# Kernel optimization log

Measured on AMD Instinct MI355X. Metric: run time of the kernel, lower is better.

The kernel has to match this reference:

```python
import jax, jax.numpy as jnp
import numpy as np

DIM, E, K, H = 1024, 8, 2, 4096

def setup_inputs() -> dict:
    key = jax.random.key(0)
    ks = jax.random.split(key, 5)
    s_in = 1.0 / np.sqrt(DIM)
    s_h = 1.0 / np.sqrt(H)
    return {
        "x": jax.random.normal(ks[0], (4, 2048, DIM), dtype=jnp.float32),
        "Wr": jax.random.normal(ks[1], (DIM, E), dtype=jnp.float32) * s_in,
        "W1": jax.random.normal(ks[2], (E, DIM, H), dtype=jnp.float32) * s_in,
        "b1": jnp.zeros((E, H), dtype=jnp.float32),
        "W2": jax.random.normal(ks[3], (E, H, DIM), dtype=jnp.float32) * s_h,
        "b2": jnp.zeros((E, DIM), dtype=jnp.float32),
    }

def reference(x, Wr, W1, b1, W2, b2):
    batch, seq, dim = x.shape
    x_flat = x.reshape(-1, dim)                      # [T, D]
    logits = x_flat @ Wr                             # [T, E]
    w, ind = jax.lax.top_k(logits, K)                # [T, K]
    w = jax.nn.softmax(w, axis=-1)
    # combine[t, e] = sum_i w[t, i] * (ind[t, i] == e)
    combine = jnp.einsum('tke,tk->te', jax.nn.one_hot(ind, E, dtype=x.dtype), w)  # [T, E]

    def body(acc, params):
        W1e, b1e, W2e, b2e, ce = params
        h = jax.nn.gelu(x_flat @ W1e + b1e, approximate=False)  # exact GELU (torch nn.GELU default)
        y = h @ W2e + b2e                                        # [T, D]
        return acc + ce[:, None] * y, None

    out0 = jnp.zeros_like(x_flat)
    out, _ = jax.lax.scan(body, out0, (W1, b1, W2, b2, combine.T))
    return out.reshape(batch, seq, dim)
```

## Files before the change

### kernel.cpp

```cpp
#include <hip/hip_runtime.h>
#include <hip/hip_bf16.h>

#define TDIM 1024
#define NEXP 8
#define NHID 4096

typedef __hip_bfloat16 bf16;
typedef __attribute__((ext_vector_type(8))) short bf16x8;
typedef __attribute__((ext_vector_type(8))) unsigned short u16x8;
typedef __attribute__((ext_vector_type(4))) float f32x4;

__device__ __forceinline__ void gload_lds16(void* lds, const void* g) {
  __builtin_amdgcn_global_load_lds(
      (const __attribute__((address_space(1))) unsigned int*)g,
      (__attribute__((address_space(3))) unsigned int*)lds, 16, 0, 0);
}

__device__ __forceinline__ unsigned short f2bf_bits(float f) {
  __hip_bfloat16 b = __float2bfloat16(f);
  unsigned short u;
  __builtin_memcpy(&u, &b, 2);
  return u;
}

__device__ __forceinline__ float bf2f(unsigned short u) {
  union { unsigned int i; float f; } c;
  c.i = ((unsigned int)u) << 16;
  return c.f;
}

__device__ __forceinline__ void cvt_chunk(const float* __restrict__ src, bf16* __restrict__ dst,
                                          int c, int kqShift, int nMask, int rowLen) {
  const int kq = c >> kqShift;
  const int n = c & nMask;
  const float* s = src + ((size_t)kq * 8) * rowLen + n;
  u16x8 o;
#pragma unroll
  for (int j = 0; j < 8; ++j) o[j] = f2bf_bits(s[(size_t)j * rowLen]);
  *reinterpret_cast<u16x8*>(dst + (size_t)c * 8) = o;
}

__global__ __launch_bounds__(256) void prep_kernel(
    const float* __restrict__ W1, bf16* __restrict__ W1C, const float* __restrict__ W2,
    bf16* __restrict__ W2C, const float* __restrict__ x, bf16* __restrict__ xb,
    const float* __restrict__ Wr, int* __restrict__ idx, float* __restrict__ wtok,
    int* __restrict__ cnt, int T) {
  const int pb = blockIdx.x;
  const int tid = threadIdx.x;
  if (pb < 8192) {
    const int id = pb * 256 + tid;
    cvt_chunk(W1, W1C, id, 12, 4095, 4096);
    cvt_chunk(W1, W1C, id + (1 << 21), 12, 4095, 4096);
    cvt_chunk(W2, W2C, id, 10, 1023, 1024);
    cvt_chunk(W2, W2C, id + (1 << 21), 10, 1023, 1024);
  } else {
    const int p = pb - 8192;
    const int wave = p * 4 + (tid >> 6);
    const int lane = tid & 63;
    if (wave >= T) return;
    const float4* xr4 = reinterpret_cast<const float4*>(x + (size_t)wave * TDIM);
    bf16* xbrow = xb + (size_t)wave * TDIM;
    float acc[NEXP];
#pragma unroll
    for (int e = 0; e < NEXP; ++e) acc[e] = 0.f;
    const float4* wr4 = reinterpret_cast<const float4*>(Wr);
#pragma unroll
    for (int i = 0; i < TDIM / 256; ++i) {
      float4 xv = xr4[lane + i * 64];
      ushort4 o;
      o.x = f2bf_bits(xv.x);
      o.y = f2bf_bits(xv.y);
      o.z = f2bf_bits(xv.z);
      o.w = f2bf_bits(xv.w);
      *reinterpret_cast<ushort4*>(xbrow + (lane + i * 64) * 4) = o;
      int row = (lane + i * 64) * 4;
#pragma unroll
      for (int j = 0; j < 4; ++j) {
        float xs = (&xv.x)[j];
        float4 wa = wr4[(row + j) * 2];
        float4 wb = wr4[(row + j) * 2 + 1];
        acc[0] += xs * wa.x;
        acc[1] += xs * wa.y;
        acc[2] += xs * wa.z;
        acc[3] += xs * wa.w;
        acc[4] += xs * wb.x;
        acc[5] += xs * wb.y;
        acc[6] += xs * wb.z;
        acc[7] += xs * wb.w;
      }
    }
#pragma unroll
    for (int e = 0; e < NEXP; ++e) {
      float v = acc[e];
#pragma unroll
      for (int s = 32; s; s >>= 1) v += __shfl_xor(v, s);
      acc[e] = v;
    }
    if (lane == 0) {
      int e0 = 0;
      float l0 = acc[0];
      for (int e = 1; e < NEXP; ++e)
        if (acc[e] > l0) { l0 = acc[e]; e0 = e; }
      int e1 = -1;
      float l1 = -INFINITY;
      for (int e = 0; e < NEXP; ++e)
        if (e != e0 && acc[e] > l1) { l1 = acc[e]; e1 = e; }
      float z = __expf(l1 - l0);
      idx[wave * 2] = e0;
      idx[wave * 2 + 1] = e1;
      wtok[wave * 2] = 1.f / (1.f + z);
      wtok[wave * 2 + 1] = z / (1.f + z);
      atomicAdd(&cnt[e0], 1);
      atomicAdd(&cnt[e1], 1);
    }
  }
}

__global__ void scan_kernel(const int* __restrict__ cnt, int* __restrict__ offs) {
  if (threadIdx.x == 0 && blockIdx.x == 0) {
    int s = 0;
    for (int e = 0; e < NEXP; ++e) { offs[e] = s; s += cnt[e]; }
  }
}

__global__ void build_perm_kernel(const int* __restrict__ idx, const int* __restrict__ offs,
                                  int* __restrict__ fill, int* __restrict__ perm,
                                  int* __restrict__ islot, int T) {
  int t = blockIdx.x * blockDim.x + threadIdx.x;
  if (t >= T) return;
#pragma unroll
  for (int k = 0; k < 2; ++k) {
    int e = idx[t * 2 + k];
    int p = offs[e] + atomicAdd(&fill[e], 1);
    perm[p] = t;
    islot[t * 2 + k] = p;
  }
}

template <int KD, int ND, bool GATHER, bool GELU>
__global__ __launch_bounds__(512, 2) void moe_gemm8(
    const bf16* __restrict__ A, const bf16* __restrict__ BC, const float* __restrict__ bias,
    const int* __restrict__ perm, const int* __restrict__ cnt, const int* __restrict__ offs,
    bf16* __restrict__ Dst, int nm, int nn) {
  __shared__ short lds[65536];

  const int nwg = NEXP * nm * nn;
  const int bid = blockIdx.x;
  const int wg = (bid & 7) * (nwg >> 3) + (bid >> 3);
  const int e = wg / (nm * nn);
  const int rem = wg % (nm * nn);
  const int mb = rem / nn, nb = rem % nn;

  const int ce = cnt[e];
  const int m0 = mb * 256;
  if (m0 >= ce) return;
  const int base = offs[e];
  const int n0 = nb * 256;
  const int tid = threadIdx.x;
  const int lane = tid & 63;
  const int wid = tid >> 6;
  const int wm = wid >> 2, wn = wid & 3;
  const int lcol = lane & 15;
  const int lkg = (lane >> 4) * 8;

  const int kxs0 = ((lkg << 1) ^ ((lcol & 7) << 4)) >> 1;
  const int kxs1 = (((lkg + 32) << 1) ^ ((lcol & 7) << 4)) >> 1;
  int aRow[4], bRow[2];
#pragma unroll
  for (int mm = 0; mm < 4; ++mm) aRow[mm] = (wm * 64 + mm * 16 + lcol) << 6;
#pragma unroll
  for (int n2 = 0; n2 < 2; ++n2) bRow[n2] = (wn * 32 + n2 * 16 + lcol) << 6;

  const bf16* aP[2][2];
  const bf16* bP[2][2];
#pragma unroll
  for (int h = 0; h < 2; ++h)
#pragma unroll
    for (int i = 0; i < 2; ++i) {
      int s = tid + i * 512;
      int srow = s >> 3;
      int ksrc = (s & 7) ^ (srow & 7);
      int grow = m0 + h * 128 + srow;
      if (grow > ce - 1) grow = ce - 1;
      size_t arow = GATHER ? (size_t)perm[base + grow] : (size_t)(base + grow);
      aP[h][i] = A + arow * KD + ksrc * 8;
      bP[h][i] = BC + (size_t)e * KD * ND + ((size_t)ksrc * ND + (n0 + h * 128 + srow)) * 8;
    }

  f32x4 acc[8][4];
#pragma unroll
  for (int m = 0; m < 8; ++m)
#pragma unroll
    for (int n = 0; n < 4; ++n) acc[m][n] = (f32x4){0.f, 0.f, 0.f, 0.f};

  bf16x8 fA[4][2], fB[2][2];

#define STAGE(SBUF, OP, HF, kA, kB)                                                  \
  {                                                                                  \
    char* sd = (char*)lds + (SBUF) * 65536 + (OP) * 32768 + (HF) * 16384 + tid * 16; \
    if (OP) {                                                                        \
      gload_lds16(sd, bP[HF][0] + (kB));                                             \
      gload_lds16(sd + 8192, bP[HF][1] + (kB));                                      \
    } else {                                                                         \
      gload_lds16(sd, aP[HF][0] + (kA));                                             \
      gload_lds16(sd + 8192, aP[HF][1] + (kA));                                      \
    }                                                                                \
  }

#define PHASE(QM, QN, RA, RB, SOP, SHF, SBUF, CBUF, kA, kB, DO_VM)                   \
  {                                                                                  \
    STAGE(SBUF, SOP, SHF, kA, kB);                                                   \
    if (DO_VM) asm volatile("s_waitcnt vmcnt(6)" ::: "memory");                      \
    __builtin_amdgcn_s_barrier();                                                    \
    asm volatile("" ::: "memory");                                                   \
    if (RA) {                                                                        \
      const short* Ab = lds + (CBUF) * 32768 + (QM) * 8192;                          \
      _Pragma("unroll") for (int mm = 0; mm < 4; ++mm) {                             \
        fA[mm][0] = *(const bf16x8*)(Ab + aRow[mm] + kxs0);                          \
        fA[mm][1] = *(const bf16x8*)(Ab + aRow[mm] + kxs1);                          \
      }                                                                              \
    }                                                                                \
    if (RB) {                                                                        \
      const short* Bb = lds + (CBUF) * 32768 + 16384 + (QN) * 8192;                  \
      _Pragma("unroll") for (int n2 = 0; n2 < 2; ++n2) {                             \
        fB[n2][0] = *(const bf16x8*)(Bb + bRow[n2] + kxs0);                          \
        fB[n2][1] = *(const bf16x8*)(Bb + bRow[n2] + kxs1);                          \
      }                                                                              \
    }                                                                                \
    asm volatile("s_waitcnt lgkmcnt(0)" ::: "memory");                               \
    __builtin_amdgcn_s_setprio(1);                                                   \
    _Pragma("unroll") for (int mm = 0; mm < 4; ++mm)                                 \
        _Pragma("unroll") for (int n2 = 0; n2 < 2; ++n2) {                           \
      acc[(QM) * 4 + mm][(QN) * 2 + n2] = __builtin_amdgcn_mfma_f32_16x16x32_bf16(   \
          fA[mm][0], fB[n2][0], acc[(QM) * 4 + mm][(QN) * 2 + n2], 0, 0, 0);         \
      acc[(QM) * 4 + mm][(QN) * 2 + n2] = __builtin_amdgcn_mfma_f32_16x16x32_bf16(   \
          fA[mm][1], fB[n2][1], acc[(QM) * 4 + mm][(QN) * 2 + n2], 0, 0, 0);         \
    }                                                                                \
    __builtin_amdgcn_s_setprio(0);                                                   \
  }

  STAGE(0, 0, 0, 0, 0);
  STAGE(0, 1, 0, 0, 0);
  STAGE(0, 0, 1, 0, 0);
  STAGE(0, 1, 1, 0, 0);

  const int NI = KD / 128;
  for (int itv = 0; itv < NI; ++itv) {
    const int k1 = itv * 128 + 64;
    int k2 = itv * 128 + 128;
    if (k2 >= KD) k2 = 0;
    const int k1B = k1 * ND, k2B = k2 * ND;
    PHASE(0, 0, 1, 1, 0, 0, 1, 0, k1, k1B, 1)
    PHASE(1, 0, 1, 0, 1, 0, 1, 0, k1, k1B, 1)
    PHASE(1, 1, 0, 1, 0, 1, 1, 0, k1, k1B, 1)
    PHASE(0, 1, 1, 0, 1, 1, 1, 0, k1, k1B, 0)
    PHASE(0, 0, 1, 1, 0, 0, 0, 1, k2, k2B, 1)
    PHASE(1, 0, 1, 0, 1, 0, 0, 1, k2, k2B, 1)
    PHASE(1, 1, 0, 1, 0, 1, 0, 1, k2, k2B, 1)
    PHASE(0, 1, 1, 0, 1, 1, 0, 1, k2, k2B, 0)
  }
#undef PHASE
#undef STAGE

  float bv[4];
#pragma unroll
  for (int ni = 0; ni < 4; ++ni)
    bv[ni] = bias[e * ND + n0 + (ni >> 1) * 128 + wn * 32 + (ni & 1) * 16 + lcol];
  const int lr4 = (lane >> 4) * 4;
#pragma unroll
  for (int mi = 0; mi < 8; ++mi) {
    const int rbase = m0 + (mi >> 2) * 128 + wm * 64 + (mi & 3) * 16 + lr4;
#pragma unroll
    for (int r = 0; r < 4; ++r) {
      int grow = rbase + r;
      if (grow < ce) {
        bf16* drow = Dst + (size_t)(base + grow) * ND;
#pragma unroll
        for (int ni = 0; ni < 4; ++ni) {
          int col = n0 + (ni >> 1) * 128 + wn * 32 + (ni & 1) * 16 + lcol;
          float v = acc[mi][ni][r] + bv[ni];
          if (GELU) v = 0.5f * v * (1.0f + erff(v * 0.70710678118654752f));
          drow[col] = __float2bfloat16(v);
        }
      }
    }
  }
}

__global__ void combine_kernel(const bf16* __restrict__ y, const int* __restrict__ islot,
                               const float* __restrict__ wtok, float* __restrict__ out) {
  const int t = blockIdx.x;
  const int d = threadIdx.x * 4;
  const int s0 = islot[t * 2], s1 = islot[t * 2 + 1];
  const float w0 = wtok[t * 2], w1 = wtok[t * 2 + 1];
  ushort4 ya = *reinterpret_cast<const ushort4*>(y + (size_t)s0 * TDIM + d);
  ushort4 yb = *reinterpret_cast<const ushort4*>(y + (size_t)s1 * TDIM + d);
  float4 o;
  o.x = w0 * bf2f(ya.x) + w1 * bf2f(yb.x);
  o.y = w0 * bf2f(ya.y) + w1 * bf2f(yb.y);
  o.z = w0 * bf2f(ya.z) + w1 * bf2f(yb.z);
  o.w = w0 * bf2f(ya.w) + w1 * bf2f(yb.w);
  *reinterpret_cast<float4*>(out + (size_t)t * TDIM + d) = o;
}

extern "C" void kernel_launch(void* const* d_in, const int* in_sizes, int n_in, void* d_out,
                              int out_size, void* d_ws, size_t ws_size, hipStream_t stream) {
  const float* x = (const float*)d_in[0];
  const float* Wr = (const float*)d_in[1];
  const float* W1 = (const float*)d_in[2];
  const float* b1 = (const float*)d_in[3];
  const float* W2 = (const float*)d_in[4];
  const float* b2 = (const float*)d_in[5];
  float* out = (float*)d_out;
  const int T = in_sizes[0] / TDIM;

  size_t off = 0;
  auto alloc = [&](size_t bytes) {
    void* q = (char*)d_ws + off;
    off += (bytes + 255) & ~(size_t)255;
    return q;
  };
  bf16* xb = (bf16*)alloc((size_t)T * TDIM * 2);
  bf16* W1C = (bf16*)alloc((size_t)NEXP * TDIM * NHID * 2);
  bf16* W2C = (bf16*)alloc((size_t)NEXP * TDIM * NHID * 2);
  bf16* h = (bf16*)alloc((size_t)2 * T * NHID * 2);
  int* idx = (int*)alloc((size_t)T * 2 * 4);
  float* wtok = (float*)alloc((size_t)T * 2 * 4);
  int* perm = (int*)alloc((size_t)T * 2 * 4);
  int* islot = (int*)alloc((size_t)T * 2 * 4);
  int* cnt = (int*)alloc(256);
  int* fill = cnt + 8;
  int* offs = cnt + 16;
  bf16* y = W1C;

  hipMemsetAsync(cnt, 0, 64, stream);

  prep_kernel<<<10240, 256, 0, stream>>>(W1, W1C, W2, W2C, x, xb, Wr, idx, wtok, cnt, T);
  scan_kernel<<<1, 64, 0, stream>>>(cnt, offs);
  build_perm_kernel<<<(T + 255) / 256, 256, 0, stream>>>(idx, offs, fill, perm, islot, T);

  moe_gemm8<TDIM, NHID, true, true><<<NEXP * 32 * 16, 512, 0, stream>>>(
      xb, W1C, b1, perm, cnt, offs, h, 32, 16);
  moe_gemm8<NHID, TDIM, false, false><<<NEXP * 32 * 4, 512, 0, stream>>>(
      h, W2C, b2, perm, cnt, offs, y, 32, 4);

  combine_kernel<<<T, 256, 0, stream>>>(y, islot, wtok, out);
}
```

Measured before the change: 794.4 us.

## Overlap W2 bf16 conversion with first expert GEMM via extra blocks

The fp32-to-bf16 conversion of W2 moves out of the prep kernel and into extra trailing workgroups of the first MoE GEMM launch, so the memory-bound conversion can run alongside the compute-bound W1 GEMM. The router logits are also restructured: x is staged in shared memory and each lane reads contiguous Wr rows, which gives more coalesced Wr loads. The risk is that conversion blocks compete with GEMM blocks for CUs and bandwidth, or are scheduled last and extend the tail. Correctness depends on those blocks finishing before the second GEMM, which stream ordering guarantees.

```diff
diff --git a/kernel.cpp b/kernel.cpp
--- a/kernel.cpp
+++ b/kernel.cpp
@@ -41,29 +41,24 @@
 }
 
 __global__ __launch_bounds__(256) void prep_kernel(
-    const float* __restrict__ W1, bf16* __restrict__ W1C, const float* __restrict__ W2,
-    bf16* __restrict__ W2C, const float* __restrict__ x, bf16* __restrict__ xb,
-    const float* __restrict__ Wr, int* __restrict__ idx, float* __restrict__ wtok,
-    int* __restrict__ cnt, int T) {
+    const float* __restrict__ W1, bf16* __restrict__ W1C, const float* __restrict__ x,
+    bf16* __restrict__ xb, const float* __restrict__ Wr, int* __restrict__ idx,
+    float* __restrict__ wtok, int* __restrict__ cnt, int T) {
+  __shared__ float xs[4][1024];
   const int pb = blockIdx.x;
   const int tid = threadIdx.x;
-  if (pb < 8192) {
+  if (pb < 4096) {
     const int id = pb * 256 + tid;
-    cvt_chunk(W1, W1C, id, 12, 4095, 4096);
-    cvt_chunk(W1, W1C, id + (1 << 21), 12, 4095, 4096);
-    cvt_chunk(W2, W2C, id, 10, 1023, 1024);
-    cvt_chunk(W2, W2C, id + (1 << 21), 10, 1023, 1024);
+#pragma unroll
+    for (int v = 0; v < 4; ++v) cvt_chunk(W1, W1C, id + v * (1 << 20), 12, 4095, 4096);
   } else {
-    const int p = pb - 8192;
+    const int p = pb - 4096;
     const int wave = p * 4 + (tid >> 6);
     const int lane = tid & 63;
     if (wave >= T) return;
+    float* xrow = xs[tid >> 6];
     const float4* xr4 = reinterpret_cast<const float4*>(x + (size_t)wave * TDIM);
     bf16* xbrow = xb + (size_t)wave * TDIM;
-    float acc[NEXP];
-#pragma unroll
-    for (int e = 0; e < NEXP; ++e) acc[e] = 0.f;
-    const float4* wr4 = reinterpret_cast<const float4*>(Wr);
 #pragma unroll
     for (int i = 0; i < TDIM / 256; ++i) {
       float4 xv = xr4[lane + i * 64];
@@ -73,21 +68,25 @@
       o.z = f2bf_bits(xv.z);
       o.w = f2bf_bits(xv.w);
       *reinterpret_cast<ushort4*>(xbrow + (lane + i * 64) * 4) = o;
-      int row = (lane + i * 64) * 4;
-#pragma unroll
-      for (int j = 0; j < 4; ++j) {
-        float xs = (&xv.x)[j];
-        float4 wa = wr4[(row + j) * 2];
-        float4 wb = wr4[(row + j) * 2 + 1];
-        acc[0] += xs * wa.x;
-        acc[1] += xs * wa.y;
-        acc[2] += xs * wa.z;
-        acc[3] += xs * wa.w;
-        acc[4] += xs * wb.x;
-        acc[5] += xs * wb.y;
-        acc[6] += xs * wb.z;
-        acc[7] += xs * wb.w;
-      }
+      *reinterpret_cast<float4*>(&xrow[(lane + i * 64) * 4]) = xv;
+    }
+    float acc[NEXP];
+#pragma unroll
+    for (int e = 0; e < NEXP; ++e) acc[e] = 0.f;
+    const float4* wr4 = reinterpret_cast<const float4*>(Wr);
+#pragma unroll
+    for (int i = 0; i < TDIM / 64; ++i) {
+      float xv = xrow[lane + i * 64];
+      float4 wa = wr4[(lane + i * 64) * 2];
+      float4 wb = wr4[(lane + i * 64) * 2 + 1];
+      acc[0] += xv * wa.x;
+      acc[1] += xv * wa.y;
+      acc[2] += xv * wa.z;
+      acc[3] += xv * wa.w;
+      acc[4] += xv * wb.x;
+      acc[5] += xv * wb.y;
+      acc[6] += xv * wb.z;
+      acc[7] += xv * wb.w;
     }
 #pragma unroll
     for (int e = 0; e < NEXP; ++e) {
@@ -137,15 +136,22 @@
   }
 }
 
-template <int KD, int ND, bool GATHER, bool GELU>
+template <int KD, int ND, bool GATHER, bool GELU, bool CONV>
 __global__ __launch_bounds__(512, 2) void moe_gemm8(
     const bf16* __restrict__ A, const bf16* __restrict__ BC, const float* __restrict__ bias,
     const int* __restrict__ perm, const int* __restrict__ cnt, const int* __restrict__ offs,
-    bf16* __restrict__ Dst, int nm, int nn) {
+    bf16* __restrict__ Dst, int nm, int nn, const float* __restrict__ Wsrc,
+    bf16* __restrict__ Wdst) {
   __shared__ short lds[65536];
 
   const int nwg = NEXP * nm * nn;
   const int bid = blockIdx.x;
+  if (CONV && bid >= nwg) {
+    const int id = (bid - nwg) * 512 + threadIdx.x;
+#pragma unroll
+    for (int v = 0; v < 8; ++v) cvt_chunk(Wsrc, Wdst, id + v * (1 << 19), 10, 1023, 1024);
+    return;
+  }
   const int wg = (bid & 7) * (nwg >> 3) + (bid >> 3);
   const int e = wg / (nm * nn);
   const int rem = wg % (nm * nn);
@@ -335,14 +341,14 @@
 
   hipMemsetAsync(cnt, 0, 64, stream);
 
-  prep_kernel<<<10240, 256, 0, stream>>>(W1, W1C, W2, W2C, x, xb, Wr, idx, wtok, cnt, T);
+  prep_kernel<<<6144, 256, 0, stream>>>(W1, W1C, x, xb, Wr, idx, wtok, cnt, T);
   scan_kernel<<<1, 64, 0, stream>>>(cnt, offs);
   build_perm_kernel<<<(T + 255) / 256, 256, 0, stream>>>(idx, offs, fill, perm, islot, T);
 
-  moe_gemm8<TDIM, NHID, true, true><<<NEXP * 32 * 16, 512, 0, stream>>>(
-      xb, W1C, b1, perm, cnt, offs, h, 32, 16);
-  moe_gemm8<NHID, TDIM, false, false><<<NEXP * 32 * 4, 512, 0, stream>>>(
-      h, W2C, b2, perm, cnt, offs, y, 32, 4);
+  moe_gemm8<TDIM, NHID, true, true, true><<<NEXP * 32 * 16 + 1024, 512, 0, stream>>>(
+      xb, W1C, b1, perm, cnt, offs, h, 32, 16, W2, W2C);
+  moe_gemm8<NHID, TDIM, false, false, false><<<NEXP * 32 * 4, 512, 0, stream>>>(
+      h, W2C, b2, perm, cnt, offs, y, 32, 4, nullptr, nullptr);
 
   combine_kernel<<<T, 256, 0, stream>>>(y, islot, wtok, out);
 }
```

Measured after the change: 775.2 us. 2.4% less time.
